# Performance work log

Hardware: AMD Instinct MI355X
Metric: run time of the kernel (lower is better)

The kernel has to match this reference:

```python
import jax, jax.numpy as jnp
import numpy as np

B, C, H, W = 32, 3, 512, 512
MIN_STR, MEAN_STR = 1.0, 5.0


def setup_inputs() -> dict:
    key = jax.random.key(0)
    k1, k2, k3, k4, k5 = jax.random.split(key, 5)
    x = jax.random.uniform(k1, (B, C, H, W), dtype=jnp.float32)  # images in [0,1]
    phases = 2.0 * jnp.pi * jax.random.uniform(k2, (B * C,), dtype=jnp.float32)
    strengths = jax.random.exponential(k3, (B, C), dtype=jnp.float32) * MEAN_STR + MIN_STR
    idx_h = jax.random.randint(k4, (B * C,), 0, H)
    idx_w = jax.random.randint(k5, (B * C,), 0, W)
    return {"x": x, "phases": phases, "strengths": strengths,
            "idx_h": idx_h, "idx_w": idx_w}


def reference(x, phases, strengths, idx_h, idx_w):
    b, c, h, w = x.shape
    # torch pairing: arange(b).repeat(c) -> i % b ; arange(c).repeat(b) -> i % c
    i = jnp.arange(b * c)
    bi = i % b
    ci = i % c
    # sparse scatter of one frequency bin per (b,c) plane
    mag = jnp.zeros_like(x).at[bi, ci, idx_h, idx_w].set(1.0)
    ph = jnp.zeros_like(x).at[bi, ci, idx_h, idx_w].set(phases)
    noise = jax.lax.complex(mag, ph)
    # symmetrize by index-reversal flip over spatial dims (as in torch .flip)
    noise = noise + jnp.flip(noise, axis=(2, 3))
    # N-D inverse FFT over spatial dims, keep real part
    w_ft = jnp.fft.ifftn(noise, axes=(2, 3)).real.astype(x.dtype)
    # L2-normalize each (b,c) plane
    norm = jnp.sqrt(jnp.sum(w_ft * w_ft, axis=(2, 3), keepdims=True))
    w_ft = w_ft / norm
    scale = max(h, w) / 32.0  # static python scalar
    out = x + scale * strengths[:, :, None, None] * w_ft
    return jnp.clip(out, 0.0, 1.0)
```

## Files before the change

### kernel.cpp

```cpp
#include <hip/hip_runtime.h>
#include <math.h>


namespace {

constexpr int H = 512, W = 512, B = 32, C = 3;
constexpr int ROWS = 32;
constexpr int TPB = 256;

__global__ __launch_bounds__(TPB) void fourier_noise_kernel(
    const float* __restrict__ xin,
    const float* __restrict__ phases,
    const float* __restrict__ strengths,
    const int* __restrict__ idx_h,
    const int* __restrict__ idx_w,
    float* __restrict__ out)
{
    const int pl = blockIdx.y;
    const int b  = pl / C;
    const int c  = pl % C;

    int d = (c - b) % 3; if (d < 0) d += 3;
    const int k = (2 * d) % 3;
    const int i = b + B * k;

    const int   h0 = idx_h[i];
    const int   w0 = idx_w[i];
    const float p  = phases[i];
    const float st = strengths[b * C + c];

    const float halfE = 0.5f * (1.0f + p * p);
    const float s1 = (((h0 & 255) == 0) && ((w0 & 255) == 0)) ? 1.0f : halfE;
    const float s2 = ((h0 == 255 || h0 == 511) && (w0 == 255 || w0 == 511)) ? 1.0f : halfE;
    const float S  = s1 + s2;
    const float g = (16.0f / 512.0f) * st * rsqrtf(S);

    const int h0r = 511 - h0;
    const int w0r = 511 - w0;
    constexpr float STEP = 6.28318530717958647692f / 512.0f;

    __shared__ float4 rowtab[ROWS];
    const int row0 = blockIdx.x * ROWS;
    for (int r = threadIdx.x; r < ROWS; r += TPB) {
        const int y = row0 + r;
        float sy1, cy1, sy2, cy2;
        sincosf(float((h0  * y) & 511) * STEP, &sy1, &cy1);
        sincosf(float((h0r * y) & 511) * STEP, &sy2, &cy2);
        rowtab[r] = make_float4(fmaf(-p, sy1, cy1), -fmaf(p, cy1, sy1),
                                fmaf(-p, sy2, cy2), -fmaf(p, cy2, sy2));
    }
    __syncthreads();

    const int xg   = (threadIdx.x & 127) << 2;
    const int rsub = threadIdx.x >> 7;

    float cx1[4], sx1[4], cx2[4], sx2[4];
#pragma unroll
    for (int j = 0; j < 4; ++j) {
        const int xx = xg + j;
        sincosf(float((w0  * xx) & 511) * STEP, &sx1[j], &cx1[j]);
        sincosf(float((w0r * xx) & 511) * STEP, &sx2[j], &cx2[j]);
    }

    const size_t plane_off = (size_t)pl * (size_t)(H * W);
#pragma unroll 4
    for (int it = 0; it < ROWS; it += 2) {
        const int r = it + rsub;
        const int y = row0 + r;
        const float4 ab = rowtab[r];
        const size_t off = plane_off + (size_t)y * W + (size_t)xg;
        const float4 vi = *reinterpret_cast<const float4*>(xin + off);
        float4 vo;
        const float* pi = &vi.x;
        float*       po = &vo.x;
#pragma unroll
        for (int j = 0; j < 4; ++j) {
            float v = cx1[j] * ab.x + sx1[j] * ab.y + cx2[j] * ab.z + sx2[j] * ab.w;
            po[j] = fminf(fmaxf(fmaf(g, v, pi[j]), 0.0f), 1.0f);
        }
        *reinterpret_cast<float4*>(out + off) = vo;
    }
}

}

extern "C" void kernel_launch(void* const* d_in, const int* in_sizes, int n_in,
                              void* d_out, int out_size, void* d_ws, size_t ws_size,
                              hipStream_t stream) {
    const float* x         = (const float*)d_in[0];
    const float* phases    = (const float*)d_in[1];
    const float* strengths = (const float*)d_in[2];
    const int*   idx_h     = (const int*)d_in[3];
    const int*   idx_w     = (const int*)d_in[4];
    float*       out       = (float*)d_out;

    dim3 grid(H / ROWS, B * C);
    fourier_noise_kernel<<<grid, dim3(TPB), 0, stream>>>(
        x, phases, strengths, idx_h, idx_w, out);
}
```

Before: 195.9 us.

## Shrink row tile, hoist input loads before sincos, use nontemporal stores

Measured after the change: 182.0 us. 1.08x faster.

```diff
diff --git a/kernel.cpp b/kernel.cpp
--- a/kernel.cpp
+++ b/kernel.cpp
@@ -5,8 +5,10 @@
 namespace {
 
 constexpr int H = 512, W = 512, B = 32, C = 3;
-constexpr int ROWS = 32;
+constexpr int ROWS = 8;
 constexpr int TPB = 256;
+
+typedef float floatx4 __attribute__((ext_vector_type(4)));
 
 __global__ __launch_bounds__(TPB) void fourier_noise_kernel(
     const float* __restrict__ xin,
@@ -39,20 +41,33 @@
     const int w0r = 511 - w0;
     constexpr float STEP = 6.28318530717958647692f / 512.0f;
 
-    __shared__ float4 rowtab[ROWS];
+    __shared__ floatx4 rowtab[ROWS];
     const int row0 = blockIdx.x * ROWS;
-    for (int r = threadIdx.x; r < ROWS; r += TPB) {
-        const int y = row0 + r;
+    if (threadIdx.x < ROWS) {
+        const int y = row0 + threadIdx.x;
         float sy1, cy1, sy2, cy2;
         sincosf(float((h0  * y) & 511) * STEP, &sy1, &cy1);
         sincosf(float((h0r * y) & 511) * STEP, &sy2, &cy2);
-        rowtab[r] = make_float4(fmaf(-p, sy1, cy1), -fmaf(p, cy1, sy1),
-                                fmaf(-p, sy2, cy2), -fmaf(p, cy2, sy2));
+        floatx4 rt;
+        rt.x = fmaf(-p, sy1, cy1);
+        rt.y = -fmaf(p, cy1, sy1);
+        rt.z = fmaf(-p, sy2, cy2);
+        rt.w = -fmaf(p, cy2, sy2);
+        rowtab[threadIdx.x] = rt;
     }
-    __syncthreads();
 
     const int xg   = (threadIdx.x & 127) << 2;
     const int rsub = threadIdx.x >> 7;
+    const size_t plane_off = (size_t)pl * (size_t)(H * W);
+
+    const size_t off0 = plane_off + (size_t)(row0 + 0 + rsub) * W + (size_t)xg;
+    const size_t off1 = plane_off + (size_t)(row0 + 2 + rsub) * W + (size_t)xg;
+    const size_t off2 = plane_off + (size_t)(row0 + 4 + rsub) * W + (size_t)xg;
+    const size_t off3 = plane_off + (size_t)(row0 + 6 + rsub) * W + (size_t)xg;
+    const floatx4 vi0 = *reinterpret_cast<const floatx4*>(xin + off0);
+    const floatx4 vi1 = *reinterpret_cast<const floatx4*>(xin + off1);
+    const floatx4 vi2 = *reinterpret_cast<const floatx4*>(xin + off2);
+    const floatx4 vi3 = *reinterpret_cast<const floatx4*>(xin + off3);
 
     float cx1[4], sx1[4], cx2[4], sx2[4];
 #pragma unroll
@@ -62,24 +77,26 @@
         sincosf(float((w0r * xx) & 511) * STEP, &sx2[j], &cx2[j]);
     }
 
-    const size_t plane_off = (size_t)pl * (size_t)(H * W);
-#pragma unroll 4
-    for (int it = 0; it < ROWS; it += 2) {
-        const int r = it + rsub;
-        const int y = row0 + r;
-        const float4 ab = rowtab[r];
-        const size_t off = plane_off + (size_t)y * W + (size_t)xg;
-        const float4 vi = *reinterpret_cast<const float4*>(xin + off);
-        float4 vo;
-        const float* pi = &vi.x;
-        float*       po = &vo.x;
-#pragma unroll
-        for (int j = 0; j < 4; ++j) {
-            float v = cx1[j] * ab.x + sx1[j] * ab.y + cx2[j] * ab.z + sx2[j] * ab.w;
-            po[j] = fminf(fmaxf(fmaf(g, v, pi[j]), 0.0f), 1.0f);
-        }
-        *reinterpret_cast<float4*>(out + off) = vo;
+    __syncthreads();
+
+#define DO_ROW(vi, off, it)                                                     \
+    {                                                                           \
+        const floatx4 ab = rowtab[(it) * 2 + rsub]; \
+        floatx4 vo;                                                             \
+        _Pragma("unroll")                                                       \
+        for (int j = 0; j < 4; ++j) {                                           \
+            float v = cx1[j] * ab.x + sx1[j] * ab.y                             \
+                    + cx2[j] * ab.z + sx2[j] * ab.w;                            \
+            vo[j] = fminf(fmaxf(fmaf(g, v, vi[j]), 0.0f), 1.0f);                \
+        }                                                                       \
+        __builtin_nontemporal_store(vo, reinterpret_cast<floatx4*>(out + off)); \
     }
+
+    DO_ROW(vi0, off0, 0)
+    DO_ROW(vi1, off1, 1)
+    DO_ROW(vi2, off2, 2)
+    DO_ROW(vi3, off3, 3)
+#undef DO_ROW
 }
 
 }
```
